# Kernel optimization log

Measured on AMD Instinct MI355X. Metric: run time of the kernel, lower is better.

Reference implementation:

```python
import jax, jax.numpy as jnp
import numpy as np

N, B, H, L0, L1, C = 196608, 4096, 230, 10, 53, 53


def setup_inputs() -> dict:
    key = jax.random.key(0)
    ks = jax.random.split(key, 12)
    x = jax.random.normal(ks[0], (N, H), jnp.float32)
    label_index = jax.random.randint(ks[1], (N,), 0, C, dtype=jnp.int32)
    rl0 = jax.random.randint(ks[2], (C, 1), 0, L0, dtype=jnp.int32)
    rl1 = jax.random.randint(ks[3], (C, 1), 0, L1, dtype=jnp.int32)
    relation_levels = jnp.concatenate([rl0, rl1], axis=1)  # [C, 2]
    # equal-size bags: 4096 bags of 48 sentences (ragged boundaries)
    scope = (jnp.arange(B + 1, dtype=jnp.int32) * (N // B))
    rel_emb0 = jax.random.normal(ks[4], (L0, H), jnp.float32)
    rel_emb1 = jax.random.normal(ks[5], (L1, H), jnp.float32)
    att_w0 = jax.random.normal(ks[6], (L0,), jnp.float32)
    att_w1 = jax.random.normal(ks[7], (L1,), jnp.float32)
    w_s = jax.random.normal(ks[8], (2, 3 * H), jnp.float32) * 0.05
    b_s = jax.random.normal(ks[9], (2, 1), jnp.float32) * 0.05
    disc_matrix = jax.random.normal(ks[10], (C, 2 * H), jnp.float32) * 0.05
    bias = jnp.zeros((C,), jnp.float32)
    return {"x": x, "rel_emb0": rel_emb0, "rel_emb1": rel_emb1,
            "att_w0": att_w0, "att_w1": att_w1, "w_s": w_s, "b_s": b_s,
            "disc_matrix": disc_matrix, "bias": bias,
            "label_index": label_index, "relation_levels": relation_levels,
            "scope": scope}


def _segment_softmax(logits, seg, num_seg):
    # logits: [N]; stable softmax within each bag (segment)
    m = jax.ops.segment_max(logits, seg, num_segments=num_seg)
    e = jnp.exp(logits - m[seg])
    z = jax.ops.segment_sum(e, seg, num_segments=num_seg)
    return e / z[seg]


def reference(x, rel_emb0, rel_emb1, att_w0, att_w1, w_s, b_s, disc_matrix,
              bias, label_index, relation_levels, scope):
    n, h = x.shape
    num_bags = scope.shape[0] - 1
    # bag id of each sentence from ragged boundaries
    seg = jnp.searchsorted(scope, jnp.arange(n, dtype=scope.dtype), side="right") - 1

    ll = relation_levels[label_index]                 # [N, 2]
    r0 = rel_emb0[ll[:, 0]]                           # [N, H]
    r1 = rel_emb1[ll[:, 1]]                           # [N, H]
    s = jnp.tanh(jnp.concatenate([x, r0, r1], axis=-1))  # [N, 3H]
    logits = w_s @ s.T + b_s                          # [2, N]

    # per-bag ragged softmax over sentences, per hierarchy level
    score = jax.vmap(lambda l: _segment_softmax(l, seg, num_bags))(logits)  # [2, N]

    # vertical (hierarchy) attention: softmax over hier per sentence, mean per bag
    v = jnp.stack([att_w0[ll[:, 0]], att_w1[ll[:, 1]]])  # [2, N]
    vsm = jax.nn.softmax(v, axis=0)                      # [2, N]
    counts = jax.ops.segment_sum(jnp.ones((n,), x.dtype), seg, num_segments=num_bags)
    layer_att = jax.vmap(lambda r: jax.ops.segment_sum(r, seg, num_segments=num_bags))(vsm) / counts  # [2, B]

    # attention-weighted bag representation: per bag, [2, len] @ [len, H]
    rep = jax.vmap(lambda sc: jax.ops.segment_sum(sc[:, None] * x, seg, num_segments=num_bags))(score)  # [2, B, H]
    tower = (layer_att[:, :, None] * rep).transpose(1, 0, 2).reshape(num_bags, 2 * h)  # [B, 2H]

    return tower @ disc_matrix.T + bias  # [B, C]
```

## Files before the change

kernel.cpp:

```cpp
#include <hip/hip_runtime.h>

#define NTOT 196608
#define BAGS 4096
#define H 230
#define H3 690
#define NC 53
#define RMAX 48
#define STR 65

__device__ __forceinline__ float fast_tanh(float x) {
    float e = __expf(2.f * x);
    float r = __builtin_amdgcn_rcpf(e + 1.f);
    return fmaf(-2.f, r, 1.f);
}

__global__ void class_table_kernel(const float* __restrict__ rel_emb0,
                                   const float* __restrict__ rel_emb1,
                                   const float* __restrict__ att_w0,
                                   const float* __restrict__ att_w1,
                                   const float* __restrict__ w_s,
                                   const float* __restrict__ b_s,
                                   const int* __restrict__ relation_levels,
                                   float* __restrict__ cls)
{
    int c = blockIdx.x;
    int lane = threadIdx.x;
    int l0 = relation_levels[c * 2 + 0];
    int l1 = relation_levels[c * 2 + 1];
    float a00 = 0.f, a01 = 0.f, a10 = 0.f, a11 = 0.f;
    for (int j = lane; j < H; j += 64) {
        float t0 = fast_tanh(rel_emb0[l0 * H + j]);
        float t1 = fast_tanh(rel_emb1[l1 * H + j]);
        a00 += w_s[0 * H3 + H + j] * t0;
        a01 += w_s[0 * H3 + 2 * H + j] * t1;
        a10 += w_s[1 * H3 + H + j] * t0;
        a11 += w_s[1 * H3 + 2 * H + j] * t1;
    }
    for (int m = 32; m; m >>= 1) {
        a00 += __shfl_xor(a00, m);
        a01 += __shfl_xor(a01, m);
        a10 += __shfl_xor(a10, m);
        a11 += __shfl_xor(a11, m);
    }
    if (lane == 0) {
        cls[0 * NC + c] = a00 + a01 + b_s[0];
        cls[1 * NC + c] = a10 + a11 + b_s[1];
        float v0 = att_w0[l0], v1 = att_w1[l1];
        float mx = fmaxf(v0, v1);
        float e0 = __expf(v0 - mx), e1 = __expf(v1 - mx);
        float rz = __builtin_amdgcn_rcpf(e0 + e1);
        cls[2 * NC + c] = e0 * rz;
        cls[3 * NC + c] = e1 * rz;
    }
}

__global__ __launch_bounds__(256, 6) void bag_kernel(
    const float* __restrict__ x,
    const float* __restrict__ w_s,
    const float* __restrict__ disc,
    const float* __restrict__ bias,
    const int* __restrict__ label_index,
    const int* __restrict__ scope,
    const float* __restrict__ cls,
    float* __restrict__ out)
{
    __shared__ __align__(16) float smem[2 * RMAX * STR];
    __shared__ __align__(16) float eArr[2 * RMAX];
    __shared__ float zsv[4];

    int b = blockIdx.x;
    int start = scope[b];
    int cnt = scope[b + 1] - start;
    int tid = threadIdx.x;
    int wave = tid >> 6;
    int lane = tid & 63;
    const float* xb = x + (long long)start * H;

    const float2* w0p = (const float2*)w_s;
    const float2* w1p = (const float2*)(w_s + H3);
    float2 w0a = w0p[lane];
    float2 w1a = w1p[lane];
    float2 w0b = make_float2(0.f, 0.f), w1b = make_float2(0.f, 0.f);
    if (lane < 51) { w0b = w0p[64 + lane]; w1b = w1p[64 + lane]; }

    float2 acc0a = make_float2(0.f, 0.f), acc0b = make_float2(0.f, 0.f);
    float2 acc1a = make_float2(0.f, 0.f), acc1b = make_float2(0.f, 0.f);

    float* dp0 = smem;
    float* dp1 = smem + RMAX * STR;

    for (int cb = 0; cb < cnt; cb += RMAX) {
        int ce = cb + RMAX; if (ce > cnt) ce = cnt;
        int rows = ce - cb;

        for (int i = cb + wave; i < ce; i += 4) {
            const float2* r2 = (const float2*)(xb + (long long)i * H);
            float2 a = r2[lane];
            float2 bb = make_float2(0.f, 0.f);
            if (lane < 51) bb = r2[64 + lane];
            float t0 = fast_tanh(a.x), t1 = fast_tanh(a.y);
            float t2 = fast_tanh(bb.x), t3 = fast_tanh(bb.y);
            int ir = i - cb;
            dp0[ir * STR + lane] = w0a.x * t0 + w0a.y * t1 + w0b.x * t2 + w0b.y * t3;
            dp1[ir * STR + lane] = w1a.x * t0 + w1a.y * t1 + w1b.x * t2 + w1b.y * t3;
        }
        __syncthreads();

        if ((wave & 1) == 0) {
            int g = wave >> 1;
            float zp = 0.f, svp = 0.f;
            if (lane < rows) {
                const float* dpr = (g ? dp1 : dp0) + lane * STR;
                float s = 0.f;
#pragma unroll
                for (int l = 0; l < 64; ++l) s += dpr[l];
                int c = label_index[start + cb + lane];
                float e = __expf(s + cls[g * NC + c]);
                eArr[2 * lane + g] = e;
                zp = e;
                svp = cls[(2 + g) * NC + c];
            }
#pragma unroll
            for (int m = 32; m; m >>= 1) {
                zp  += __shfl_xor(zp, m);
                svp += __shfl_xor(svp, m);
            }
            if (lane == 0) {
                if (cb == 0) { zsv[2 * g] = zp;  zsv[2 * g + 1] = svp; }
                else         { zsv[2 * g] += zp; zsv[2 * g + 1] += svp; }
            }
        }
        __syncthreads();

        for (int i = cb + wave; i < ce; i += 4) {
            const float2* r2 = (const float2*)(xb + (long long)i * H);
            float2 a = r2[lane];
            float2 bb = make_float2(0.f, 0.f);
            if (lane < 51) bb = r2[64 + lane];
            int ir = i - cb;
            float e0 = eArr[2 * ir];
            float e1 = eArr[2 * ir + 1];
            acc0a.x = fmaf(e0, a.x,  acc0a.x); acc0a.y = fmaf(e0, a.y,  acc0a.y);
            acc0b.x = fmaf(e0, bb.x, acc0b.x); acc0b.y = fmaf(e0, bb.y, acc0b.y);
            acc1a.x = fmaf(e1, a.x,  acc1a.x); acc1a.y = fmaf(e1, a.y,  acc1a.y);
            acc1b.x = fmaf(e1, bb.x, acc1b.x); acc1b.y = fmaf(e1, bb.y, acc1b.y);
        }
    }

    float2* pw = (float2*)(smem + wave * 464);
    pw[lane]       = acc0a;
    pw[115 + lane] = acc1a;
    if (lane < 51) {
        pw[64 + lane]       = acc0b;
        pw[115 + 64 + lane] = acc1b;
    }
    __syncthreads();

    float rc = __builtin_amdgcn_rcpf((float)cnt);
    float s0 = zsv[1] * rc * __builtin_amdgcn_rcpf(zsv[0]);
    float s1 = zsv[3] * rc * __builtin_amdgcn_rcpf(zsv[2]);

    float* t01 = smem + 1856;
    for (int t = tid; t < 2 * H; t += 256) {
        float s = smem[t] + smem[464 + t] + smem[928 + t] + smem[1392 + t];
        t01[t] = s * (t < H ? s0 : s1);
    }
    __syncthreads();

    int q = tid & 3;
    int c = tid >> 2;
    if (c < NC) {
        const float4* drow4 = (const float4*)(disc + c * (2 * H));
        const float4* t4 = (const float4*)t01;
        float acc = 0.f;
        for (int k = q; k < 115; k += 4) {
            float4 dv = drow4[k];
            float4 tv = t4[k];
            acc += dv.x * tv.x + dv.y * tv.y + dv.z * tv.z + dv.w * tv.w;
        }
        acc += __shfl_down(acc, 2, 4);
        acc += __shfl_down(acc, 1, 4);
        if (q == 0) out[b * NC + c] = acc + bias[c];
    }
}

extern "C" void kernel_launch(void* const* d_in, const int* in_sizes, int n_in,
                              void* d_out, int out_size, void* d_ws, size_t ws_size,
                              hipStream_t stream) {
    const float* x               = (const float*)d_in[0];
    const float* rel_emb0        = (const float*)d_in[1];
    const float* rel_emb1        = (const float*)d_in[2];
    const float* att_w0          = (const float*)d_in[3];
    const float* att_w1          = (const float*)d_in[4];
    const float* w_s             = (const float*)d_in[5];
    const float* b_s             = (const float*)d_in[6];
    const float* disc            = (const float*)d_in[7];
    const float* bias            = (const float*)d_in[8];
    const int*   label_index     = (const int*)d_in[9];
    const int*   relation_levels = (const int*)d_in[10];
    const int*   scope           = (const int*)d_in[11];
    float* out = (float*)d_out;
    float* cls = (float*)d_ws;

    class_table_kernel<<<NC, 64, 0, stream>>>(rel_emb0, rel_emb1, att_w0, att_w1,
                                              w_s, b_s, relation_levels, cls);
    bag_kernel<<<BAGS, 256, 0, stream>>>(x, w_s, disc, bias, label_index, scope,
                                         cls, out);
}
```

Baseline: 322.4 us.

## Keep bag rows in registers and reduce dot partials with ds_swizzle

Each wave now holds its assigned x rows in registers (up to 12 float2 pairs) across the logit, softmax and weighted-sum phases. Previously every row was read from global memory a second time for the weighted sum. The per-row dot products are reduced within groups of 8 lanes using ds_swizzle, so LDS holds 8 partials per row instead of 64. The class table is staged in LDS, and one wave handles both hierarchy levels of the softmax. The cost is higher register pressure, which may reduce occupancy under the existing launch bounds.

```diff
diff --git a/kernel.cpp b/kernel.cpp
--- a/kernel.cpp
+++ b/kernel.cpp
@@ -5,8 +5,9 @@
 #define H 230
 #define H3 690
 #define NC 53
-#define RMAX 48
-#define STR 65
+
+#define SWZ_ADD(v, pat) \
+    ((v) + __int_as_float(__builtin_amdgcn_ds_swizzle(__float_as_int(v), (pat))))
 
 __device__ __forceinline__ float fast_tanh(float x) {
     float e = __expf(2.f * x);
@@ -64,90 +65,124 @@
     const float* __restrict__ cls,
     float* __restrict__ out)
 {
-    __shared__ __align__(16) float smem[2 * RMAX * STR];
-    __shared__ __align__(16) float eArr[2 * RMAX];
-    __shared__ float zsv[4];
+    __shared__ __align__(16) float ldsA[2320];
+    __shared__ __align__(16) float clsL[4 * NC];
+    __shared__ __align__(8)  float2 eL[48];
+    __shared__ float zsL[2];
 
     int b = blockIdx.x;
-    int start = scope[b];
-    int cnt = scope[b + 1] - start;
     int tid = threadIdx.x;
     int wave = tid >> 6;
     int lane = tid & 63;
-    const float* xb = x + (long long)start * H;
+
+    if (tid < 4 * NC) clsL[tid] = cls[tid];
+
+    int sstart = __builtin_amdgcn_readfirstlane(scope[b]);
+    int cnt    = __builtin_amdgcn_readfirstlane(scope[b + 1]) - sstart;
+    int swave  = __builtin_amdgcn_readfirstlane(wave);
+
+    int li = (lane < 51) ? lane : 50;
 
     const float2* w0p = (const float2*)w_s;
     const float2* w1p = (const float2*)(w_s + H3);
-    float2 w0a = w0p[lane];
-    float2 w1a = w1p[lane];
+    float2 w0a = w0p[lane], w1a = w1p[lane];
     float2 w0b = make_float2(0.f, 0.f), w1b = make_float2(0.f, 0.f);
     if (lane < 51) { w0b = w0p[64 + lane]; w1b = w1p[64 + lane]; }
 
+    float2* dpF2 = (float2*)ldsA;
+
     float2 acc0a = make_float2(0.f, 0.f), acc0b = make_float2(0.f, 0.f);
     float2 acc1a = make_float2(0.f, 0.f), acc1b = make_float2(0.f, 0.f);
-
-    float* dp0 = smem;
-    float* dp1 = smem + RMAX * STR;
-
-    for (int cb = 0; cb < cnt; cb += RMAX) {
-        int ce = cb + RMAX; if (ce > cnt) ce = cnt;
-        int rows = ce - cb;
-
-        for (int i = cb + wave; i < ce; i += 4) {
-            const float2* r2 = (const float2*)(xb + (long long)i * H);
-            float2 a = r2[lane];
-            float2 bb = make_float2(0.f, 0.f);
-            if (lane < 51) bb = r2[64 + lane];
-            float t0 = fast_tanh(a.x), t1 = fast_tanh(a.y);
-            float t2 = fast_tanh(bb.x), t3 = fast_tanh(bb.y);
-            int ir = i - cb;
-            dp0[ir * STR + lane] = w0a.x * t0 + w0a.y * t1 + w0b.x * t2 + w0b.y * t3;
-            dp1[ir * STR + lane] = w1a.x * t0 + w1a.y * t1 + w1b.x * t2 + w1b.y * t3;
+    float z0t = 0.f, z1t = 0.f, sv0t = 0.f, sv1t = 0.f;
+
+    for (int cb = 0; cb < cnt; cb += 48) {
+        int rows = cnt - cb; if (rows > 48) rows = 48;
+
+        float2 ra[12], rb[12];
+#pragma unroll
+        for (int t = 0; t < 12; ++t) {
+            int r = swave + 4 * t;
+            if (r < rows) {
+                int roff = (sstart + cb + r) * H;
+                const float2* rp = (const float2*)(x + roff);
+                float2 a  = rp[lane];
+                float2 bb = rp[64 + li];
+                ra[t] = a; rb[t] = bb;
+                float t0 = fast_tanh(a.x),  t1 = fast_tanh(a.y);
+                float t2 = fast_tanh(bb.x), t3 = fast_tanh(bb.y);
+                float d0 = w0a.x * t0 + w0a.y * t1 + w0b.x * t2 + w0b.y * t3;
+                float d1 = w1a.x * t0 + w1a.y * t1 + w1b.x * t2 + w1b.y * t3;
+                d0 = SWZ_ADD(d0, 0x041F);
+                d0 = SWZ_ADD(d0, 0x081F);
+                d0 = SWZ_ADD(d0, 0x101F);
+                d1 = SWZ_ADD(d1, 0x041F);
+                d1 = SWZ_ADD(d1, 0x081F);
+                d1 = SWZ_ADD(d1, 0x101F);
+                if ((lane & 7) == 0)
+                    dpF2[r * 9 + (lane >> 3)] = make_float2(d0, d1);
+            }
         }
         __syncthreads();
 
-        if ((wave & 1) == 0) {
-            int g = wave >> 1;
-            float zp = 0.f, svp = 0.f;
-            if (lane < rows) {
-                const float* dpr = (g ? dp1 : dp0) + lane * STR;
-                float s = 0.f;
+        if (tid < 64) {
+            int r = tid;
+            float e0 = 0.f, e1 = 0.f, sp0 = 0.f, sp1 = 0.f;
+            if (r < rows) {
+                int c = label_index[sstart + cb + r];
+                float d0 = 0.f, d1 = 0.f;
 #pragma unroll
-                for (int l = 0; l < 64; ++l) s += dpr[l];
-                int c = label_index[start + cb + lane];
-                float e = __expf(s + cls[g * NC + c]);
-                eArr[2 * lane + g] = e;
-                zp = e;
-                svp = cls[(2 + g) * NC + c];
+                for (int p = 0; p < 8; ++p) {
+                    float2 v = dpF2[r * 9 + p];
+                    d0 += v.x; d1 += v.y;
+                }
+                e0 = __expf(d0 + clsL[c]);
+                e1 = __expf(d1 + clsL[NC + c]);
+                sp0 = clsL[2 * NC + c];
+                sp1 = clsL[3 * NC + c];
+                eL[r] = make_float2(e0, e1);
             }
+            z0t += e0; z1t += e1; sv0t += sp0; sv1t += sp1;
+        }
+        __syncthreads();
+
 #pragma unroll
-            for (int m = 32; m; m >>= 1) {
-                zp  += __shfl_xor(zp, m);
-                svp += __shfl_xor(svp, m);
+        for (int t = 0; t < 12; ++t) {
+            int r = swave + 4 * t;
+            if (r < rows) {
+                float2 e = eL[r];
+                acc0a.x = fmaf(e.x, ra[t].x, acc0a.x);
+                acc0a.y = fmaf(e.x, ra[t].y, acc0a.y);
+                acc0b.x = fmaf(e.x, rb[t].x, acc0b.x);
+                acc0b.y = fmaf(e.x, rb[t].y, acc0b.y);
+                acc1a.x = fmaf(e.y, ra[t].x, acc1a.x);
+                acc1a.y = fmaf(e.y, ra[t].y, acc1a.y);
+                acc1b.x = fmaf(e.y, rb[t].x, acc1b.x);
+                acc1b.y = fmaf(e.y, rb[t].y, acc1b.y);
             }
-            if (lane == 0) {
-                if (cb == 0) { zsv[2 * g] = zp;  zsv[2 * g + 1] = svp; }
-                else         { zsv[2 * g] += zp; zsv[2 * g + 1] += svp; }
-            }
-        }
-        __syncthreads();
-
-        for (int i = cb + wave; i < ce; i += 4) {
-            const float2* r2 = (const float2*)(xb + (long long)i * H);
-            float2 a = r2[lane];
-            float2 bb = make_float2(0.f, 0.f);
-            if (lane < 51) bb = r2[64 + lane];
-            int ir = i - cb;
-            float e0 = eArr[2 * ir];
-            float e1 = eArr[2 * ir + 1];
-            acc0a.x = fmaf(e0, a.x,  acc0a.x); acc0a.y = fmaf(e0, a.y,  acc0a.y);
-            acc0b.x = fmaf(e0, bb.x, acc0b.x); acc0b.y = fmaf(e0, bb.y, acc0b.y);
-            acc1a.x = fmaf(e1, a.x,  acc1a.x); acc1a.y = fmaf(e1, a.y,  acc1a.y);
-            acc1b.x = fmaf(e1, bb.x, acc1b.x); acc1b.y = fmaf(e1, bb.y, acc1b.y);
-        }
-    }
-
-    float2* pw = (float2*)(smem + wave * 464);
+        }
+    }
+
+    if (tid < 64) {
+        z0t  = SWZ_ADD(z0t,  0x041F); z0t  = SWZ_ADD(z0t,  0x081F);
+        z0t  = SWZ_ADD(z0t,  0x101F); z0t  = SWZ_ADD(z0t,  0x201F);
+        z0t  = SWZ_ADD(z0t,  0x401F); z0t  += __shfl_xor(z0t, 32);
+        z1t  = SWZ_ADD(z1t,  0x041F); z1t  = SWZ_ADD(z1t,  0x081F);
+        z1t  = SWZ_ADD(z1t,  0x101F); z1t  = SWZ_ADD(z1t,  0x201F);
+        z1t  = SWZ_ADD(z1t,  0x401F); z1t  += __shfl_xor(z1t, 32);
+        sv0t = SWZ_ADD(sv0t, 0x041F); sv0t = SWZ_ADD(sv0t, 0x081F);
+        sv0t = SWZ_ADD(sv0t, 0x101F); sv0t = SWZ_ADD(sv0t, 0x201F);
+        sv0t = SWZ_ADD(sv0t, 0x401F); sv0t += __shfl_xor(sv0t, 32);
+        sv1t = SWZ_ADD(sv1t, 0x041F); sv1t = SWZ_ADD(sv1t, 0x081F);
+        sv1t = SWZ_ADD(sv1t, 0x101F); sv1t = SWZ_ADD(sv1t, 0x201F);
+        sv1t = SWZ_ADD(sv1t, 0x401F); sv1t += __shfl_xor(sv1t, 32);
+        if (lane == 0) {
+            float rc = __builtin_amdgcn_rcpf((float)cnt);
+            zsL[0] = sv0t * rc * __builtin_amdgcn_rcpf(z0t);
+            zsL[1] = sv1t * rc * __builtin_amdgcn_rcpf(z1t);
+        }
+    }
+
+    float2* pw = (float2*)(ldsA + wave * 464);
     pw[lane]       = acc0a;
     pw[115 + lane] = acc1a;
     if (lane < 51) {
@@ -156,13 +191,10 @@
     }
     __syncthreads();
 
-    float rc = __builtin_amdgcn_rcpf((float)cnt);
-    float s0 = zsv[1] * rc * __builtin_amdgcn_rcpf(zsv[0]);
-    float s1 = zsv[3] * rc * __builtin_amdgcn_rcpf(zsv[2]);
-
-    float* t01 = smem + 1856;
+    float s0 = zsL[0], s1 = zsL[1];
+    float* t01 = ldsA + 1856;
     for (int t = tid; t < 2 * H; t += 256) {
-        float s = smem[t] + smem[464 + t] + smem[928 + t] + smem[1392 + t];
+        float s = ldsA[t] + ldsA[464 + t] + ldsA[928 + t] + ldsA[1392 + t];
         t01[t] = s * (t < H ? s0 : s1);
     }
     __syncthreads();
```

Measured after the change: 309.6 us. 4.0% less time.
